# Kernel optimization log

Measured on AMD Instinct MI355X. Metric: run time of the kernel, lower is better.

## Reference

```python
import jax, jax.numpy as jnp
import numpy as np

NUM_NODES = 50000
NUM_EDGES = 1600000
IN_C = 512
OUT_C = 512


def setup_inputs() -> dict:
    key = jax.random.key(0)
    k1, k2, k3, k4 = jax.random.split(key, 4)
    x = jax.random.normal(k1, (NUM_NODES, IN_C), dtype=jnp.float32)
    edge_index = jax.random.randint(k2, (2, NUM_EDGES), 0, NUM_NODES, dtype=jnp.int64)
    # nn.Linear params (kaiming-uniform-ish scale)
    lim = 1.0 / np.sqrt(IN_C)
    W = jax.random.uniform(k3, (OUT_C, IN_C), dtype=jnp.float32, minval=-lim, maxval=lim)
    b = jax.random.uniform(k4, (OUT_C,), dtype=jnp.float32, minval=-lim, maxval=lim)
    return {"x": x, "edge_index": edge_index, "W": W, "b": b}


def reference(x, edge_index, W, b):
    num_nodes = x.shape[0]
    src = edge_index[0]
    tar = edge_index[1]
    # dense layer: feat = x @ W^T + b  -> [N, out_c]
    feat = jnp.einsum('ni,oi->no', x, W) + b
    # degree: scatter_add of ones over src, plus self-loop term (+1)
    ones_e = jnp.ones((src.shape[0],), dtype=feat.dtype)
    deg = jax.ops.segment_sum(ones_e, src, num_segments=num_nodes) + 1.0
    deg_inv_sqrt = jnp.where(deg > 0, deg ** -0.5, 0.0)
    # per-edge normalized weight
    w = deg_inv_sqrt[src] * deg_inv_sqrt[tar]  # [E]
    # sparse-coo matmul: out[src] += w * feat[tar]
    msgs = w[:, None] * feat[tar]  # [E, out_c]
    out = jax.ops.segment_sum(msgs, src, num_segments=num_nodes)
    # self contribution: feat * deg^{-1}
    out = out + feat * (1.0 / deg)[:, None]
    return out
```

## Files before the change

### kernel.cpp

```cpp
#include <hip/hip_runtime.h>

#define IN_C 512
#define OUT_C 512

typedef __attribute__((ext_vector_type(4))) float f32x4;
typedef __attribute__((ext_vector_type(8))) short bf16x8;

__device__ __forceinline__ unsigned short f2bf_rne(float f) {
    unsigned int u = __float_as_uint(f);
    u += 0x7fffu + ((u >> 16) & 1u);
    return (unsigned short)(u >> 16);
}
__device__ __forceinline__ float bflo(unsigned int u) { return __uint_as_float(u << 16); }
__device__ __forceinline__ float bfhi(unsigned int u) { return __uint_as_float(u & 0xffff0000u); }

__global__ void k_convert(const float* __restrict__ in, unsigned short* __restrict__ out, int n8) {
    int i = blockIdx.x * blockDim.x + threadIdx.x;
    if (i >= n8) return;
    const float4* in4 = (const float4*)in;
    float4 a = in4[i * 2], b = in4[i * 2 + 1];
    uint4 o;
    o.x = (unsigned)f2bf_rne(a.x) | ((unsigned)f2bf_rne(a.y) << 16);
    o.y = (unsigned)f2bf_rne(a.z) | ((unsigned)f2bf_rne(a.w) << 16);
    o.z = (unsigned)f2bf_rne(b.x) | ((unsigned)f2bf_rne(b.y) << 16);
    o.w = (unsigned)f2bf_rne(b.z) | ((unsigned)f2bf_rne(b.w) << 16);
    *(uint4*)&out[(size_t)i * 8] = o;
}

__global__ void k_degree(const int* __restrict__ src, int E, int* __restrict__ deg) {
    int e = blockIdx.x * blockDim.x + threadIdx.x;
    if (e < E) atomicAdd(&deg[src[e]], 1);
}

__global__ __launch_bounds__(1024) void k_scan1(const int* __restrict__ deg, int N,
                                                int* __restrict__ row_start,
                                                int* __restrict__ bsum,
                                                float* __restrict__ dinv) {
    __shared__ int wsum[16];
    int t = threadIdx.x;
    int wave = t >> 6, lane = t & 63;
    int i = blockIdx.x * 1024 + t;
    int v = (i < N) ? deg[i] : 0;
    if (i < N) dinv[i] = rsqrtf((float)(v + 1));
    int s = v;
#pragma unroll
    for (int off = 1; off < 64; off <<= 1) {
        int u = __shfl_up(s, off, 64);
        if (lane >= off) s += u;
    }
    if (lane == 63) wsum[wave] = s;
    __syncthreads();
    if (wave == 0 && lane < 16) {
        int ws = wsum[lane];
#pragma unroll
        for (int off = 1; off < 16; off <<= 1) {
            int u = __shfl_up(ws, off, 64);
            if (lane >= off) ws += u;
        }
        wsum[lane] = ws;
    }
    __syncthreads();
    int waveOff = (wave == 0) ? 0 : wsum[wave - 1];
    if (i < N) row_start[i] = s - v + waveOff;
    if (t == 0) bsum[blockIdx.x] = wsum[15];
}

__global__ void k_scan2(int* __restrict__ bsum, int nb) {
    int lane = threadIdx.x & 63;
    int v = (lane < nb) ? bsum[lane] : 0;
    int s = v;
#pragma unroll
    for (int off = 1; off < 64; off <<= 1) {
        int u = __shfl_up(s, off, 64);
        if (lane >= off) s += u;
    }
    if (lane < nb) bsum[lane] = s - v;
    if (lane == 63) bsum[nb] = s;
}

__global__ void k_scan3(int* __restrict__ row_start, const int* __restrict__ bsum, int N, int nb) {
    int i = blockIdx.x * blockDim.x + threadIdx.x;
    if (i < N) row_start[i] += bsum[i >> 10];
    if (i == 0) row_start[N] = bsum[nb];
}

__global__ void k_fill(const int* __restrict__ src, const int* __restrict__ tar, int E,
                       const int* __restrict__ row_start, int* __restrict__ fill,
                       int* __restrict__ csr_tar) {
    int e = blockIdx.x * blockDim.x + threadIdx.x;
    if (e < E) {
        int s = src[e];
        int p = atomicAdd(&fill[s], 1);
        csr_tar[row_start[s] + p] = tar[e];
    }
}

__global__ __launch_bounds__(256) void k_gemm_mfma(const unsigned short* __restrict__ xb,
                                                   const unsigned short* __restrict__ wb,
                                                   const float* __restrict__ bias,
                                                   unsigned short* __restrict__ featb, int N) {
    int tid = threadIdx.x;
    int wave = tid >> 6, lane = tid & 63;
    int wr = wave >> 1, wc = wave & 1;
    int rowBase = blockIdx.y * 128 + wr * 64;
    int colBase = blockIdx.x * 128 + wc * 64;
    int r0 = lane & 15;
    int kg = lane >> 4;

    f32x4 acc[4][4];
#pragma unroll
    for (int mi = 0; mi < 4; ++mi)
#pragma unroll
        for (int ni = 0; ni < 4; ++ni)
            acc[mi][ni] = (f32x4){0.f, 0.f, 0.f, 0.f};

    for (int k0 = 0; k0 < IN_C; k0 += 32) {
        bf16x8 a[4], b[4];
#pragma unroll
        for (int mi = 0; mi < 4; ++mi) {
            int r = rowBase + mi * 16 + r0;
            if (r > N - 1) r = N - 1;
            a[mi] = *(const bf16x8*)&xb[(size_t)r * IN_C + k0 + kg * 8];
        }
#pragma unroll
        for (int ni = 0; ni < 4; ++ni) {
            int ccol = colBase + ni * 16 + r0;
            b[ni] = *(const bf16x8*)&wb[(size_t)ccol * IN_C + k0 + kg * 8];
        }
#pragma unroll
        for (int mi = 0; mi < 4; ++mi)
#pragma unroll
            for (int ni = 0; ni < 4; ++ni)
                acc[mi][ni] = __builtin_amdgcn_mfma_f32_16x16x32_bf16(a[mi], b[ni], acc[mi][ni], 0, 0, 0);
    }

    float bv[4];
#pragma unroll
    for (int ni = 0; ni < 4; ++ni) bv[ni] = bias[colBase + ni * 16 + r0];

#pragma unroll
    for (int mi = 0; mi < 4; ++mi) {
#pragma unroll
        for (int reg = 0; reg < 4; ++reg) {
            int grow = rowBase + mi * 16 + kg * 4 + reg;
            if (grow < N) {
#pragma unroll
                for (int ni = 0; ni < 4; ++ni) {
                    float v = acc[mi][ni][reg] + bv[ni];
                    featb[(size_t)grow * OUT_C + colBase + ni * 16 + r0] = f2bf_rne(v);
                }
            }
        }
    }
}

__device__ __forceinline__ void acc8(float* accf, uint4 v, float wgt) {
    accf[0] += wgt * bflo(v.x); accf[1] += wgt * bfhi(v.x);
    accf[2] += wgt * bflo(v.y); accf[3] += wgt * bfhi(v.y);
    accf[4] += wgt * bflo(v.z); accf[5] += wgt * bfhi(v.z);
    accf[6] += wgt * bflo(v.w); accf[7] += wgt * bfhi(v.w);
}

__global__ __launch_bounds__(256) void k_aggregate(const unsigned short* __restrict__ featb,
                                                   const float* __restrict__ dinv,
                                                   const int* __restrict__ row_start,
                                                   const int* __restrict__ csr_tar,
                                                   float* __restrict__ out, int N) {
    int wave = threadIdx.x >> 6, lane = threadIdx.x & 63;
    int n = blockIdx.x * 4 + wave;
    if (n >= N) return;
    float din = dinv[n];
    int rs = row_start[n], re = row_start[n + 1];
    float accf[8] = {0.f, 0.f, 0.f, 0.f, 0.f, 0.f, 0.f, 0.f};

    for (int base = rs; base < re; base += 64) {
        int m = re - base;
        if (m > 64) m = 64;
        int t_l = 0;
        float w_l = 0.f;
        if (lane < m) {
            t_l = csr_tar[base + lane];
            w_l = din * dinv[t_l];
        }
        int j = 0;
        for (; j + 4 <= m; j += 4) {
            int t0 = __shfl(t_l, j, 64),     t1 = __shfl(t_l, j + 1, 64);
            int t2 = __shfl(t_l, j + 2, 64), t3 = __shfl(t_l, j + 3, 64);
            float w0 = __shfl(w_l, j, 64),     w1 = __shfl(w_l, j + 1, 64);
            float w2 = __shfl(w_l, j + 2, 64), w3 = __shfl(w_l, j + 3, 64);
            uint4 v0 = *(const uint4*)&featb[(size_t)t0 * OUT_C + lane * 8];
            uint4 v1 = *(const uint4*)&featb[(size_t)t1 * OUT_C + lane * 8];
            uint4 v2 = *(const uint4*)&featb[(size_t)t2 * OUT_C + lane * 8];
            uint4 v3 = *(const uint4*)&featb[(size_t)t3 * OUT_C + lane * 8];
            acc8(accf, v0, w0);
            acc8(accf, v1, w1);
            acc8(accf, v2, w2);
            acc8(accf, v3, w3);
        }
        for (; j < m; ++j) {
            int t = __shfl(t_l, j, 64);
            float w = __shfl(w_l, j, 64);
            uint4 v = *(const uint4*)&featb[(size_t)t * OUT_C + lane * 8];
            acc8(accf, v, w);
        }
    }

    {
        uint4 v = *(const uint4*)&featb[(size_t)n * OUT_C + lane * 8];
        acc8(accf, v, din * din);
    }
    float4 o0 = {accf[0], accf[1], accf[2], accf[3]};
    float4 o1 = {accf[4], accf[5], accf[6], accf[7]};
    *(float4*)&out[(size_t)n * OUT_C + lane * 8] = o0;
    *(float4*)&out[(size_t)n * OUT_C + lane * 8 + 4] = o1;
}

extern "C" void kernel_launch(void* const* d_in, const int* in_sizes, int n_in,
                              void* d_out, int out_size, void* d_ws, size_t ws_size,
                              hipStream_t stream) {
    const float* x    = (const float*)d_in[0];
    const int*   ei   = (const int*)d_in[1];
    const float* W    = (const float*)d_in[2];
    const float* bias = (const float*)d_in[3];
    float* out = (float*)d_out;

    int N = in_sizes[0] / IN_C;
    int E = in_sizes[1] / 2;
    const int* src = ei;
    const int* tar = ei + E;
    int nb = (N + 1023) >> 10;

    char* ws = (char*)d_ws;
    unsigned short* featb = (unsigned short*)ws;
    size_t off = (size_t)N * OUT_C * sizeof(unsigned short);
    unsigned short* xb = (unsigned short*)(ws + off);
    size_t xb_off = off;
    off += (size_t)N * IN_C * sizeof(unsigned short);
    unsigned short* wb = (unsigned short*)(ws + off);
    off += (size_t)OUT_C * IN_C * sizeof(unsigned short);
    float* dinv = (float*)(ws + off);      off += (size_t)N * sizeof(float);
    int* deg = (int*)(ws + off);           off += (size_t)N * sizeof(int);
    int* fill = (int*)(ws + off);          off += (size_t)N * sizeof(int);
    int* row_start = (int*)(ws + off);     off += (size_t)(N + 1) * sizeof(int);
    int* bsum = (int*)(ws + off);          off += (size_t)(nb + 1) * sizeof(int);
    int* csr_tar = (int*)(ws + xb_off);

    int n8x = N * IN_C / 8;
    k_convert<<<(n8x + 255) / 256, 256, 0, stream>>>(x, xb, n8x);
    int n8w = OUT_C * IN_C / 8;
    k_convert<<<(n8w + 255) / 256, 256, 0, stream>>>(W, wb, n8w);
    dim3 g(OUT_C / 128, (N + 127) / 128);
    k_gemm_mfma<<<g, 256, 0, stream>>>(xb, wb, bias, featb, N);

    (void)hipMemsetAsync(deg, 0, 2 * (size_t)N * sizeof(int), stream);
    k_degree<<<(E + 255) / 256, 256, 0, stream>>>(src, E, deg);
    k_scan1<<<nb, 1024, 0, stream>>>(deg, N, row_start, bsum, dinv);
    k_scan2<<<1, 64, 0, stream>>>(bsum, nb);
    k_scan3<<<(N + 255) / 256, 256, 0, stream>>>(row_start, bsum, N, nb);
    k_fill<<<(E + 255) / 256, 256, 0, stream>>>(src, tar, E, row_start, fill, csr_tar);

    k_aggregate<<<(N + 3) / 4, 256, 0, stream>>>(featb, dinv, row_start, csr_tar, out, N);
}
```

Baseline: 681.1 us.

## Fuse x bf16 conversion into LDS-tiled GEMM and merge scan passes

The GEMM now reads fp32 x directly, converts it to bf16 while staging 128x32 tiles of A and B in shared memory, and the MFMA waves read their fragments from LDS. This removes the separate x conversion kernel and its 50MB bf16 intermediate round trip, and it shares global loads across waves. The scan2 kernel is removed: scan3 now computes each block's prefix with a wavefront reduction over the block sums and writes E as the final row_start. The costs are extra __syncthreads per k-step with no double buffering, and the fp32 x being read by each of the 4 column blocks.

```diff
diff --git a/kernel.cpp b/kernel.cpp
--- a/kernel.cpp
+++ b/kernel.cpp
@@ -65,23 +65,17 @@
     if (t == 0) bsum[blockIdx.x] = wsum[15];
 }
 
-__global__ void k_scan2(int* __restrict__ bsum, int nb) {
+__global__ void k_scan3(int* __restrict__ row_start, const int* __restrict__ bsum,
+                        int N, int E) {
     int lane = threadIdx.x & 63;
-    int v = (lane < nb) ? bsum[lane] : 0;
-    int s = v;
-#pragma unroll
-    for (int off = 1; off < 64; off <<= 1) {
-        int u = __shfl_up(s, off, 64);
-        if (lane >= off) s += u;
-    }
-    if (lane < nb) bsum[lane] = s - v;
-    if (lane == 63) bsum[nb] = s;
-}
-
-__global__ void k_scan3(int* __restrict__ row_start, const int* __restrict__ bsum, int N, int nb) {
-    int i = blockIdx.x * blockDim.x + threadIdx.x;
-    if (i < N) row_start[i] += bsum[i >> 10];
-    if (i == 0) row_start[N] = bsum[nb];
+    int chunk = blockIdx.x >> 2;
+    int v = (lane < chunk) ? bsum[lane] : 0;
+#pragma unroll
+    for (int off = 1; off < 64; off <<= 1)
+        v += __shfl_xor(v, off, 64);
+    int i = blockIdx.x * 256 + threadIdx.x;
+    if (i < N) row_start[i] += v;
+    if (i == 0) row_start[N] = E;
 }
 
 __global__ void k_fill(const int* __restrict__ src, const int* __restrict__ tar, int E,
@@ -95,17 +89,18 @@
     }
 }
 
-__global__ __launch_bounds__(256) void k_gemm_mfma(const unsigned short* __restrict__ xb,
-                                                   const unsigned short* __restrict__ wb,
-                                                   const float* __restrict__ bias,
-                                                   unsigned short* __restrict__ featb, int N) {
+__global__ __launch_bounds__(256) void k_gemm_fused(const float* __restrict__ x,
+                                                    const unsigned short* __restrict__ wb,
+                                                    const float* __restrict__ bias,
+                                                    unsigned short* __restrict__ featb, int N) {
+    __shared__ unsigned short As[128 * 40];
+    __shared__ unsigned short Bs[128 * 40];
     int tid = threadIdx.x;
     int wave = tid >> 6, lane = tid & 63;
     int wr = wave >> 1, wc = wave & 1;
-    int rowBase = blockIdx.y * 128 + wr * 64;
-    int colBase = blockIdx.x * 128 + wc * 64;
-    int r0 = lane & 15;
-    int kg = lane >> 4;
+    int rowBase = blockIdx.y * 128;
+    int colBase = blockIdx.x * 128;
+    int r0 = lane & 15, kg = lane >> 4;
 
     f32x4 acc[4][4];
 #pragma unroll
@@ -115,39 +110,56 @@
             acc[mi][ni] = (f32x4){0.f, 0.f, 0.f, 0.f};
 
     for (int k0 = 0; k0 < IN_C; k0 += 32) {
+#pragma unroll
+        for (int i = 0; i < 4; ++i) {
+            int idx = tid + i * 256;
+            int row = idx >> 3, q = idx & 7;
+            int grow = rowBase + row;
+            if (grow > N - 1) grow = N - 1;
+            float4 v = *(const float4*)&x[(size_t)grow * IN_C + k0 + q * 4];
+            ushort4 b4;
+            b4.x = f2bf_rne(v.x); b4.y = f2bf_rne(v.y);
+            b4.z = f2bf_rne(v.z); b4.w = f2bf_rne(v.w);
+            *(ushort4*)&As[row * 40 + q * 4] = b4;
+        }
+#pragma unroll
+        for (int i = 0; i < 2; ++i) {
+            int idx = tid + i * 256;
+            int col = idx >> 2, q = idx & 3;
+            uint4 v = *(const uint4*)&wb[(size_t)(colBase + col) * IN_C + k0 + q * 8];
+            *(uint4*)&Bs[col * 40 + q * 8] = v;
+        }
+        __syncthreads();
+
         bf16x8 a[4], b[4];
 #pragma unroll
-        for (int mi = 0; mi < 4; ++mi) {
-            int r = rowBase + mi * 16 + r0;
-            if (r > N - 1) r = N - 1;
-            a[mi] = *(const bf16x8*)&xb[(size_t)r * IN_C + k0 + kg * 8];
-        }
-#pragma unroll
-        for (int ni = 0; ni < 4; ++ni) {
-            int ccol = colBase + ni * 16 + r0;
-            b[ni] = *(const bf16x8*)&wb[(size_t)ccol * IN_C + k0 + kg * 8];
-        }
+        for (int mi = 0; mi < 4; ++mi)
+            a[mi] = *(const bf16x8*)&As[(wr * 64 + mi * 16 + r0) * 40 + kg * 8];
+#pragma unroll
+        for (int ni = 0; ni < 4; ++ni)
+            b[ni] = *(const bf16x8*)&Bs[(wc * 64 + ni * 16 + r0) * 40 + kg * 8];
 #pragma unroll
         for (int mi = 0; mi < 4; ++mi)
 #pragma unroll
             for (int ni = 0; ni < 4; ++ni)
                 acc[mi][ni] = __builtin_amdgcn_mfma_f32_16x16x32_bf16(a[mi], b[ni], acc[mi][ni], 0, 0, 0);
+        __syncthreads();
     }
 
     float bv[4];
 #pragma unroll
-    for (int ni = 0; ni < 4; ++ni) bv[ni] = bias[colBase + ni * 16 + r0];
+    for (int ni = 0; ni < 4; ++ni) bv[ni] = bias[colBase + wc * 64 + ni * 16 + r0];
 
 #pragma unroll
     for (int mi = 0; mi < 4; ++mi) {
 #pragma unroll
         for (int reg = 0; reg < 4; ++reg) {
-            int grow = rowBase + mi * 16 + kg * 4 + reg;
+            int grow = rowBase + wr * 64 + mi * 16 + kg * 4 + reg;
             if (grow < N) {
 #pragma unroll
                 for (int ni = 0; ni < 4; ++ni) {
                     float v = acc[mi][ni][reg] + bv[ni];
-                    featb[(size_t)grow * OUT_C + colBase + ni * 16 + r0] = f2bf_rne(v);
+                    featb[(size_t)grow * OUT_C + colBase + wc * 64 + ni * 16 + r0] = f2bf_rne(v);
                 }
             }
         }
@@ -233,9 +245,6 @@
     char* ws = (char*)d_ws;
     unsigned short* featb = (unsigned short*)ws;
     size_t off = (size_t)N * OUT_C * sizeof(unsigned short);
-    unsigned short* xb = (unsigned short*)(ws + off);
-    size_t xb_off = off;
-    off += (size_t)N * IN_C * sizeof(unsigned short);
     unsigned short* wb = (unsigned short*)(ws + off);
     off += (size_t)OUT_C * IN_C * sizeof(unsigned short);
     float* dinv = (float*)(ws + off);      off += (size_t)N * sizeof(float);
@@ -243,20 +252,17 @@
     int* fill = (int*)(ws + off);          off += (size_t)N * sizeof(int);
     int* row_start = (int*)(ws + off);     off += (size_t)(N + 1) * sizeof(int);
     int* bsum = (int*)(ws + off);          off += (size_t)(nb + 1) * sizeof(int);
-    int* csr_tar = (int*)(ws + xb_off);
-
-    int n8x = N * IN_C / 8;
-    k_convert<<<(n8x + 255) / 256, 256, 0, stream>>>(x, xb, n8x);
+    int* csr_tar = (int*)(ws + off);       off += (size_t)E * sizeof(int);
+
     int n8w = OUT_C * IN_C / 8;
     k_convert<<<(n8w + 255) / 256, 256, 0, stream>>>(W, wb, n8w);
     dim3 g(OUT_C / 128, (N + 127) / 128);
-    k_gemm_mfma<<<g, 256, 0, stream>>>(xb, wb, bias, featb, N);
+    k_gemm_fused<<<g, 256, 0, stream>>>(x, wb, bias, featb, N);
 
     (void)hipMemsetAsync(deg, 0, 2 * (size_t)N * sizeof(int), stream);
     k_degree<<<(E + 255) / 256, 256, 0, stream>>>(src, E, deg);
     k_scan1<<<nb, 1024, 0, stream>>>(deg, N, row_start, bsum, dinv);
-    k_scan2<<<1, 64, 0, stream>>>(bsum, nb);
-    k_scan3<<<(N + 255) / 256, 256, 0, stream>>>(row_start, bsum, N, nb);
+    k_scan3<<<(N + 255) / 256, 256, 0, stream>>>(row_start, bsum, N, E);
     k_fill<<<(E + 255) / 256, 256, 0, stream>>>(src, tar, E, row_start, fill, csr_tar);
 
     k_aggregate<<<(N + 3) / 4, 256, 0, stream>>>(featb, dinv, row_start, csr_tar, out, N);
```

Result: faster. 635.3 us (-6.7%).
